# Optimization experiments

Hardware: AMD Instinct MI355X
Metric: run time of the kernel (lower is better)

Reference implementation:

```python
import jax, jax.numpy as jnp
import numpy as np

SMOOTH = 9.0
EPS = 1e-8
LEAK = 0.1  # LeakyReLU slope used by SCAN_attention


def setup_inputs() -> dict:
    key = jax.random.key(0)
    k1, k2, k3, k4 = jax.random.split(key, 4)
    n_img, n_reg, d = 256, 36, 1024
    n_cap, max_w = 256, 60
    imgs = jax.random.normal(k1, (n_img, n_reg, d), dtype=jnp.float32)
    caps = jax.random.normal(k2, (n_cap, max_w, d), dtype=jnp.float32)
    img_lens = jax.random.randint(k3, (n_img,), 1, n_reg + 1, dtype=jnp.int32)
    cap_lens = jax.random.randint(k4, (n_cap,), 5, max_w + 1, dtype=jnp.int32)
    return {"imgs": imgs, "caps": caps, "img_lens": img_lens, "cap_lens": cap_lens}


def reference(imgs, caps, img_lens, cap_lens):
    # imgs: (I, R, D); caps: (C, W, D); cap_lens: (C,)
    C, W, D = caps.shape
    mask = (jnp.arange(W)[None, :] < cap_lens[:, None]).astype(caps.dtype)  # (C, W)
    # Zero padded words: equivalent to the per-caption slicing in the torch loop
    q = caps * mask[:, :, None]

    # SCAN attention, vectorized over captions and images.
    # raw scores: context . query^T  -> (C, I, W, R)
    s = jnp.einsum('cwd,ird->ciwr', q, imgs)
    s = jnp.where(s >= 0, s, LEAK * s)  # LeakyReLU(0.1)
    # l2norm over the word dim (padded words contribute exactly 0)
    norm = jnp.sqrt(jnp.sum(s * s, axis=2, keepdims=True)) + EPS
    s = s / norm
    attn = jax.nn.softmax(s * SMOOTH, axis=3)  # softmax over regions
    wctx = jnp.einsum('ciwr,ird->ciwd', attn, imgs)  # (C, I, W, D)

    # cosine similarity over feature dim
    w12 = jnp.einsum('cwd,ciwd->ciw', q, wctx)
    w1 = jnp.sqrt(jnp.sum(q * q, axis=-1))[:, None, :]          # (C, 1, W)
    w2 = jnp.sqrt(jnp.sum(wctx * wctx, axis=-1))                # (C, I, W)
    sim = w12 / jnp.maximum(w1 * w2, EPS)                       # (C, I, W)

    # masked mean over valid words (matches per-caption mean over n_word)
    col = jnp.sum(sim * mask[:, None, :], axis=2) / cap_lens.astype(sim.dtype)[:, None]
    return col.T  # (n_image, n_caption)
```

## Files before the change

kernel.cpp:

```cpp
#include <hip/hip_runtime.h>


#define NIMG 256
#define NREG 36
#define DIM 1024
#define NCAP 256
#define MAXW 60
#define WPAD 64

typedef short bf16x8 __attribute__((ext_vector_type(8)));
typedef float f32x4 __attribute__((ext_vector_type(4)));

__device__ __forceinline__ unsigned short f2bf(float f) {
  unsigned u = __float_as_uint(f);
  u += 0x7FFF + ((u >> 16) & 1);
  return (unsigned short)(u >> 16);
}

__global__ void k_prep_w1(const float* __restrict__ caps, const int* __restrict__ cap_lens,
                          float* __restrict__ w1) {
  const int bid = blockIdx.x;
  const int c = bid >> 6;
  const int w = bid & 63;
  const int t = threadIdx.x;
  const bool valid = (w < MAXW) && (w < cap_lens[c]);
  float4 v = make_float4(0.f, 0.f, 0.f, 0.f);
  if (valid) v = *reinterpret_cast<const float4*>(caps + ((size_t)c * MAXW + w) * DIM + t * 4);
  float ss = v.x * v.x + v.y * v.y + v.z * v.z + v.w * v.w;
#pragma unroll
  for (int m = 1; m <= 32; m <<= 1) ss += __shfl_xor(ss, m);
  __shared__ float part[4];
  if ((t & 63) == 0) part[t >> 6] = ss;
  __syncthreads();
  if (t == 0) w1[bid] = sqrtf(part[0] + part[1] + part[2] + part[3]);
}

__global__ void k_prep_caps_frag(const float* __restrict__ caps, const int* __restrict__ cap_lens,
                                 unsigned short* __restrict__ qbfF) {
  const int k32 = blockIdx.x;
  const int c = blockIdx.y;
  const int t = threadIdx.x;
  const int mt = t >> 6;
  const int lane = t & 63;
  const int m = mt * 16 + (lane & 15);
  const int k0 = k32 * 32 + (lane >> 4) * 8;
  const int clen = cap_lens[c];
  float4 v0 = make_float4(0.f, 0.f, 0.f, 0.f), v1 = v0;
  if (m < clen && m < MAXW) {
    const float* src = caps + ((size_t)c * MAXW + m) * DIM + k0;
    v0 = *reinterpret_cast<const float4*>(src);
    v1 = *reinterpret_cast<const float4*>(src + 4);
  }
  ushort4 o0, o1;
  o0.x = f2bf(v0.x); o0.y = f2bf(v0.y); o0.z = f2bf(v0.z); o0.w = f2bf(v0.w);
  o1.x = f2bf(v1.x); o1.y = f2bf(v1.y); o1.z = f2bf(v1.z); o1.w = f2bf(v1.w);
  unsigned short* dst = qbfF + ((size_t)(((c * 32 + k32) * 4 + mt) * 64 + lane)) * 8;
  *reinterpret_cast<ushort4*>(dst) = o0;
  *reinterpret_cast<ushort4*>(dst + 4) = o1;
}

__global__ void k_prep_imgs_frag(const float* __restrict__ imgs,
                                 unsigned short* __restrict__ ibfF) {
  const int k32 = blockIdx.x;
  const int i = blockIdx.y;
  const int t = threadIdx.x;
  const int nt = t >> 6;
  const int lane = t & 63;
  const int r = nt * 16 + (lane & 15);
  const int k0 = k32 * 32 + (lane >> 4) * 8;
  float4 v0 = make_float4(0.f, 0.f, 0.f, 0.f), v1 = v0;
  if (r < NREG) {
    const float* src = imgs + ((size_t)i * NREG + r) * DIM + k0;
    v0 = *reinterpret_cast<const float4*>(src);
    v1 = *reinterpret_cast<const float4*>(src + 4);
  }
  ushort4 o0, o1;
  o0.x = f2bf(v0.x); o0.y = f2bf(v0.y); o0.z = f2bf(v0.z); o0.w = f2bf(v0.w);
  o1.x = f2bf(v1.x); o1.y = f2bf(v1.y); o1.z = f2bf(v1.z); o1.w = f2bf(v1.w);
  unsigned short* dst = ibfF + ((size_t)(((i * 32 + k32) * 3 + nt) * 64 + lane)) * 8;
  *reinterpret_cast<ushort4*>(dst) = o0;
  *reinterpret_cast<ushort4*>(dst + 4) = o1;
}

__global__ void k_gram_mfma(const float* __restrict__ imgs,
                            const unsigned short* __restrict__ ibfF,
                            unsigned short* __restrict__ gbf,
                            float* __restrict__ gdiag) {
  const int i = blockIdx.x;
  const int lane = threadIdx.x & 63;
  const int l15 = lane & 15;
  const int quad = lane >> 4;

  float* dg = gdiag + (size_t)i * 48;
#pragma unroll
  for (int r0 = 0; r0 < 36; r0 += 4) {
    const int r = r0 + quad;
    const float* row = imgs + ((size_t)i * NREG + r) * DIM;
    float ss = 0.f;
#pragma unroll
    for (int p = 0; p < 16; ++p) {
      float4 v = *reinterpret_cast<const float4*>(row + p * 64 + l15 * 4);
      ss += v.x * v.x + v.y * v.y + v.z * v.z + v.w * v.w;
    }
    ss += __shfl_xor(ss, 1); ss += __shfl_xor(ss, 2);
    ss += __shfl_xor(ss, 4); ss += __shfl_xor(ss, 8);
    if (l15 == 0) dg[r] = ss;
  }
  if (lane < 12) dg[36 + lane] = 0.f;

  const unsigned short* base = ibfF + ((size_t)i * 32 * 3) * 512 + lane * 8;
  const f32x4 zero4 = {0.f, 0.f, 0.f, 0.f};
  f32x4 acc[3][3];
#pragma unroll
  for (int na = 0; na < 3; ++na)
#pragma unroll
    for (int nb = 0; nb < 3; ++nb) acc[na][nb] = zero4;
  bf16x8 f[2][3];
#pragma unroll
  for (int nt = 0; nt < 3; ++nt)
    f[0][nt] = *reinterpret_cast<const bf16x8*>(base + (size_t)nt * 512);
#pragma unroll
  for (int k32 = 0; k32 < 32; ++k32) {
    if (k32 + 1 < 32) {
      const int nb_ = (k32 + 1) & 1;
#pragma unroll
      for (int nt = 0; nt < 3; ++nt)
        f[nb_][nt] = *reinterpret_cast<const bf16x8*>(base + ((size_t)(k32 + 1) * 3 + nt) * 512);
    }
    const int b = k32 & 1;
#pragma unroll
    for (int na = 0; na < 3; ++na)
#pragma unroll
      for (int nb = 0; nb < 3; ++nb)
        acc[na][nb] = __builtin_amdgcn_mfma_f32_16x16x32_bf16(f[b][na], f[b][nb], acc[na][nb], 0, 0, 0);
  }
  unsigned short* g = gbf + (size_t)i * (48 * 64);
#pragma unroll
  for (int na = 0; na < 3; ++na)
#pragma unroll
    for (int nb = 0; nb < 3; ++nb)
#pragma unroll
      for (int rg = 0; rg < 4; ++rg) {
        const int r = na * 16 + quad * 4 + rg;
        const int c = nb * 16 + l15;
        g[r * 64 + c] = (r == c) ? (unsigned short)0 : f2bf(acc[na][nb][rg]);
      }
  for (int idx = lane; idx < 96; idx += 64) {
    const int r = idx >> 1, half = idx & 1;
    *reinterpret_cast<uint4*>(g + r * 64 + 48 + half * 8) = make_uint4(0, 0, 0, 0);
  }
}

template <int MLIM>
__device__ __forceinline__ void kloopT(const unsigned short* __restrict__ aBase,
                                       const unsigned short* __restrict__ bBase,
                                       f32x4 (&acc)[4][3]) {
  bf16x8 fa[3][MLIM], fb[3][3];
  auto load = [&](int k32, int buf) __attribute__((always_inline)) {
#pragma unroll
    for (int nt = 0; nt < 3; ++nt)
      fb[buf][nt] = *reinterpret_cast<const bf16x8*>(bBase + ((size_t)k32 * 3 + nt) * 512);
#pragma unroll
    for (int mt = 0; mt < MLIM; ++mt)
      fa[buf][mt] = *reinterpret_cast<const bf16x8*>(aBase + ((size_t)k32 * 4 + mt) * 512);
  };
  auto compute = [&](int buf) __attribute__((always_inline)) {
#pragma unroll
    for (int mt = 0; mt < MLIM; ++mt)
#pragma unroll
      for (int nt = 0; nt < 3; ++nt)
        acc[mt][nt] = __builtin_amdgcn_mfma_f32_16x16x32_bf16(fa[buf][mt], fb[buf][nt], acc[mt][nt], 0, 0, 0);
  };
  load(0, 0);
  load(1, 1);
#pragma unroll
  for (int k32 = 0; k32 < 32; ++k32) {
    if (k32 + 2 < 32) load(k32 + 2, (k32 + 2) % 3);
    __builtin_amdgcn_sched_barrier(0);
    compute(k32 % 3);
  }
}

__launch_bounds__(256, 3)
__global__ void k_main(const unsigned short* __restrict__ qbfF,
                       const unsigned short* __restrict__ ibfF,
                       const float* __restrict__ w1,
                       const unsigned short* __restrict__ gbf,
                       const float* __restrict__ gdiag,
                       const int* __restrict__ cap_lens,
                       float* __restrict__ out) {
  __shared__ struct {
    unsigned short attn[4][64 * 64];
    float w12[4][64];
    float w2d[4][64];
    float w2x[4][64];
  } lds;
  const int tid = threadIdx.x;
  const int lane = tid & 63;
  const int wv = tid >> 6;
  const int l15 = lane & 15;
  const int quad = lane >> 4;
  const int flat = blockIdx.y * (NIMG / 2) + blockIdx.x;
  const int xcd = flat & 7;
  const int idx = flat >> 3;
  const int bx = xcd * 16 + (idx & 15);
  const int by = idx >> 4;
  const int i0 = bx * 2;
  const int c = by * 2 + (wv & 1);
  const int img = i0 + (wv >> 1);
  const int clen = cap_lens[c];
  const int mlim = (clen + 15) >> 4;

  f32x4 acc[4][3];
  const f32x4 zero4 = {0.f, 0.f, 0.f, 0.f};
#pragma unroll
  for (int mt = 0; mt < 4; ++mt)
#pragma unroll
    for (int nt = 0; nt < 3; ++nt) acc[mt][nt] = zero4;

  const unsigned short* aBase = qbfF + ((size_t)c * 32 * 4) * 512 + lane * 8;
  const unsigned short* bBase = ibfF + ((size_t)img * 32 * 3) * 512 + lane * 8;

  switch (mlim) {
    case 1: kloopT<1>(aBase, bBase, acc); break;
    case 2: kloopT<2>(aBase, bBase, acc); break;
    case 3: kloopT<3>(aBase, bBase, acc); break;
    default: kloopT<4>(aBase, bBase, acc); break;
  }

  {
    uint4* ab = reinterpret_cast<uint4*>(&lds.attn[wv][0]);
    const uint4 z4 = make_uint4(0, 0, 0, 0);
    for (int j = lane; j < 512; j += 64) ab[j] = z4;
  }

  const int lo = l15 & 7, hi = l15 >> 3;
  const float* dg = gdiag + (size_t)img * 48;
  const float d0 = dg[l15];
  const float d1 = dg[16 + l15];
  const float d2 = dg[32 + l15];

  float scale[3];
#pragma unroll
  for (int nt = 0; nt < 3; ++nt) {
    float p = 0.f;
#pragma unroll
    for (int mt = 0; mt < 4; ++mt)
      if (mt < mlim)
#pragma unroll
        for (int rg = 0; rg < 4; ++rg) {
          float s = acc[mt][nt][rg];
          float l = s < 0.f ? 0.1f * s : s;
          p += l * l;
        }
    p += __shfl_xor(p, 16);
    p += __shfl_xor(p, 32);
    scale[nt] = 9.0f / (sqrtf(p) + 1e-8f);
  }
  const bool vr2 = (l15 < 4);
#pragma unroll
  for (int mt = 0; mt < 4; ++mt) {
    if (mt >= mlim) continue;
#pragma unroll
    for (int rg = 0; rg < 4; ++rg) {
      const float s0 = acc[mt][0][rg];
      const float s1 = acc[mt][1][rg];
      const float s2 = acc[mt][2][rg];
      const float t0 = (s0 < 0.f ? 0.1f * s0 : s0) * scale[0];
      const float t1 = (s1 < 0.f ? 0.1f * s1 : s1) * scale[1];
      const float t2 = (s2 < 0.f ? 0.1f * s2 : s2) * scale[2];
      float mx = fmaxf(t0, t1);
      if (vr2) mx = fmaxf(mx, t2);
      mx = fmaxf(mx, __shfl_xor(mx, 1));
      mx = fmaxf(mx, __shfl_xor(mx, 2));
      mx = fmaxf(mx, __shfl_xor(mx, 4));
      mx = fmaxf(mx, __shfl_xor(mx, 8));
      const float e0 = __expf(t0 - mx);
      const float e1 = __expf(t1 - mx);
      const float e2 = vr2 ? __expf(t2 - mx) : 0.f;
      float sm = e0 + e1 + e2;
      sm += __shfl_xor(sm, 1);
      sm += __shfl_xor(sm, 2);
      sm += __shfl_xor(sm, 4);
      sm += __shfl_xor(sm, 8);
      const float inv = 1.0f / sm;
      const float a0 = e0 * inv, a1 = e1 * inv, a2 = e2 * inv;
      float wp = a0 * s0 + a1 * s1 + a2 * s2;
      float dd = a0 * a0 * d0 + a1 * a1 * d1 + a2 * a2 * d2;
      wp += __shfl_xor(wp, 1); wp += __shfl_xor(wp, 2);
      wp += __shfl_xor(wp, 4); wp += __shfl_xor(wp, 8);
      dd += __shfl_xor(dd, 1); dd += __shfl_xor(dd, 2);
      dd += __shfl_xor(dd, 4); dd += __shfl_xor(dd, 8);
      const int w = mt * 16 + quad * 4 + rg;
      const int w7 = w & 7;
      unsigned short* arow = &lds.attn[wv][w * 64];
      arow[(((0 + hi) ^ w7) << 3) + lo] = f2bf(a0);
      arow[(((2 + hi) ^ w7) << 3) + lo] = f2bf(a1);
      arow[(((4 + hi) ^ w7) << 3) + lo] = f2bf(a2);
      if (l15 == 0) { lds.w12[wv][w] = wp; lds.w2d[wv][w] = dd; }
    }
  }
  bf16x8 gfrag[3][2];
#pragma unroll
  for (int nt = 0; nt < 3; ++nt)
#pragma unroll
    for (int ks = 0; ks < 2; ++ks)
      gfrag[nt][ks] = *reinterpret_cast<const bf16x8*>(
          gbf + ((size_t)img * 48 + nt * 16 + l15) * 64 + ((ks * 4 + quad) << 3));
#pragma unroll
  for (int mt = 0; mt < 4; ++mt) {
    if (mt >= mlim) continue;
    bf16x8 af[2];
#pragma unroll
    for (int ks = 0; ks < 2; ++ks)
      af[ks] = *reinterpret_cast<const bf16x8*>(
          &lds.attn[wv][(mt * 16 + l15) * 64 + (((ks * 4 + quad) ^ (l15 & 7)) << 3)]);
    f32x4 Y[3] = {zero4, zero4, zero4};
#pragma unroll
    for (int nt = 0; nt < 3; ++nt)
#pragma unroll
      for (int ks = 0; ks < 2; ++ks)
        Y[nt] = __builtin_amdgcn_mfma_f32_16x16x32_bf16(af[ks], gfrag[nt][ks], Y[nt], 0, 0, 0);
#pragma unroll
    for (int rg = 0; rg < 4; ++rg) {
      const int w = mt * 16 + quad * 4 + rg;
      const int w7 = w & 7;
      float p = 0.f;
#pragma unroll
      for (int nt = 0; nt < 3; ++nt) {
        const unsigned short b = lds.attn[wv][w * 64 + (((nt * 2 + hi) ^ w7) << 3) + lo];
        p += __uint_as_float((unsigned)b << 16) * Y[nt][rg];
      }
      p += __shfl_xor(p, 1); p += __shfl_xor(p, 2);
      p += __shfl_xor(p, 4); p += __shfl_xor(p, 8);
      if (l15 == 0) lds.w2x[wv][w] = p;
    }
  }
  float simv = 0.f;
  if (lane < clen) {
    const float w2sq = fmaxf(lds.w2x[wv][lane] + lds.w2d[wv][lane], 0.f);
    const float w2v = sqrtf(w2sq);
    const float w12v = lds.w12[wv][lane];
    const float w1v = w1[(size_t)c * WPAD + lane];
    simv = w12v / fmaxf(w1v * w2v, 1e-8f);
  }
  simv += __shfl_xor(simv, 1);
  simv += __shfl_xor(simv, 2);
  simv += __shfl_xor(simv, 4);
  simv += __shfl_xor(simv, 8);
  simv += __shfl_xor(simv, 16);
  simv += __shfl_xor(simv, 32);
  if (lane == 0) out[(size_t)img * NCAP + c] = simv / (float)clen;
}

extern "C" void kernel_launch(void* const* d_in, const int* in_sizes, int n_in,
                              void* d_out, int out_size, void* d_ws, size_t ws_size,
                              hipStream_t stream) {
  const float* imgs = (const float*)d_in[0];
  const float* caps = (const float*)d_in[1];
  const int* cap_lens = (const int*)d_in[3];
  float* out = (float*)d_out;

  char* ws = (char*)d_ws;
  const size_t QBF_B = (size_t)NCAP * 32 * 4 * 512 * 2;
  const size_t IBF_B = (size_t)NIMG * 32 * 3 * 512 * 2;
  const size_t W1_B = (size_t)NCAP * WPAD * 4;
  const size_t GBF_B = (size_t)NIMG * 48 * 64 * 2;
  unsigned short* qbfF = (unsigned short*)ws;
  unsigned short* ibfF = (unsigned short*)(ws + QBF_B);
  float* w1 = (float*)(ws + QBF_B + IBF_B);
  unsigned short* gbf = (unsigned short*)(ws + QBF_B + IBF_B + W1_B);
  float* gdiag = (float*)(ws + QBF_B + IBF_B + W1_B + GBF_B);

  k_prep_w1<<<NCAP * WPAD, 256, 0, stream>>>(caps, cap_lens, w1);
  k_prep_caps_frag<<<dim3(32, NCAP), 256, 0, stream>>>(caps, cap_lens, qbfF);
  k_prep_imgs_frag<<<dim3(32, NIMG), 192, 0, stream>>>(imgs, ibfF);
  k_gram_mfma<<<NIMG, 64, 0, stream>>>(imgs, ibfF, gbf, gdiag);
  k_main<<<dim3(NIMG / 2, NCAP / 2), 256, 0, stream>>>(qbfF, ibfF, w1, gbf, gdiag, cap_lens, out);
}
```

Before: 597.7 us.

## Transpose MFMA operands so softmax over regions runs in-lane with fewer shuffles

```diff
diff --git a/kernel.cpp b/kernel.cpp
--- a/kernel.cpp
+++ b/kernel.cpp
@@ -154,7 +154,7 @@
 template <int MLIM>
 __device__ __forceinline__ void kloopT(const unsigned short* __restrict__ aBase,
                                        const unsigned short* __restrict__ bBase,
-                                       f32x4 (&acc)[4][3]) {
+                                       f32x4 (&acc)[3][4]) {
   bf16x8 fa[3][MLIM], fb[3][3];
   auto load = [&](int k32, int buf) __attribute__((always_inline)) {
 #pragma unroll
@@ -169,7 +169,7 @@
     for (int mt = 0; mt < MLIM; ++mt)
 #pragma unroll
       for (int nt = 0; nt < 3; ++nt)
-        acc[mt][nt] = __builtin_amdgcn_mfma_f32_16x16x32_bf16(fa[buf][mt], fb[buf][nt], acc[mt][nt], 0, 0, 0);
+        acc[nt][mt] = __builtin_amdgcn_mfma_f32_16x16x32_bf16(fb[buf][nt], fa[buf][mt], acc[nt][mt], 0, 0, 0);
   };
   load(0, 0);
   load(1, 1);
@@ -211,12 +211,12 @@
   const int clen = cap_lens[c];
   const int mlim = (clen + 15) >> 4;
 
-  f32x4 acc[4][3];
+  f32x4 acc[3][4];
   const f32x4 zero4 = {0.f, 0.f, 0.f, 0.f};
 #pragma unroll
-  for (int mt = 0; mt < 4; ++mt)
-#pragma unroll
-    for (int nt = 0; nt < 3; ++nt) acc[mt][nt] = zero4;
+  for (int nt = 0; nt < 3; ++nt)
+#pragma unroll
+    for (int mt = 0; mt < 4; ++mt) acc[nt][mt] = zero4;
 
   const unsigned short* aBase = qbfF + ((size_t)c * 32 * 4) * 512 + lane * 8;
   const unsigned short* bBase = ibfF + ((size_t)img * 32 * 3) * 512 + lane * 8;
@@ -234,72 +234,70 @@
     for (int j = lane; j < 512; j += 64) ab[j] = z4;
   }
 
-  const int lo = l15 & 7, hi = l15 >> 3;
   const float* dg = gdiag + (size_t)img * 48;
-  const float d0 = dg[l15];
-  const float d1 = dg[16 + l15];
-  const float d2 = dg[32 + l15];
-
-  float scale[3];
-#pragma unroll
-  for (int nt = 0; nt < 3; ++nt) {
-    float p = 0.f;
-#pragma unroll
-    for (int mt = 0; mt < 4; ++mt)
-      if (mt < mlim)
-#pragma unroll
-        for (int rg = 0; rg < 4; ++rg) {
-          float s = acc[mt][nt][rg];
-          float l = s < 0.f ? 0.1f * s : s;
+  float dv[3][4];
+#pragma unroll
+  for (int nt = 0; nt < 3; ++nt)
+#pragma unroll
+    for (int rg = 0; rg < 4; ++rg)
+      dv[nt][rg] = dg[nt * 16 + quad * 4 + rg];
+
+  float scale[3][4];
+#pragma unroll
+  for (int nt = 0; nt < 3; ++nt)
+#pragma unroll
+    for (int rg = 0; rg < 4; ++rg) {
+      float p = 0.f;
+#pragma unroll
+      for (int mt = 0; mt < 4; ++mt)
+        if (mt < mlim) {
+          const float s = acc[nt][mt][rg];
+          const float l = s < 0.f ? 0.1f * s : s;
           p += l * l;
         }
-    p += __shfl_xor(p, 16);
-    p += __shfl_xor(p, 32);
-    scale[nt] = 9.0f / (sqrtf(p) + 1e-8f);
-  }
-  const bool vr2 = (l15 < 4);
+      p += __shfl_xor(p, 1); p += __shfl_xor(p, 2);
+      p += __shfl_xor(p, 4); p += __shfl_xor(p, 8);
+      scale[nt][rg] = 9.0f / (sqrtf(p) + 1e-8f);
+    }
+
+  float a_all[4][3][4];
+  float inv4[4];
 #pragma unroll
   for (int mt = 0; mt < 4; ++mt) {
     if (mt >= mlim) continue;
-#pragma unroll
-    for (int rg = 0; rg < 4; ++rg) {
-      const float s0 = acc[mt][0][rg];
-      const float s1 = acc[mt][1][rg];
-      const float s2 = acc[mt][2][rg];
-      const float t0 = (s0 < 0.f ? 0.1f * s0 : s0) * scale[0];
-      const float t1 = (s1 < 0.f ? 0.1f * s1 : s1) * scale[1];
-      const float t2 = (s2 < 0.f ? 0.1f * s2 : s2) * scale[2];
-      float mx = fmaxf(t0, t1);
-      if (vr2) mx = fmaxf(mx, t2);
-      mx = fmaxf(mx, __shfl_xor(mx, 1));
-      mx = fmaxf(mx, __shfl_xor(mx, 2));
-      mx = fmaxf(mx, __shfl_xor(mx, 4));
-      mx = fmaxf(mx, __shfl_xor(mx, 8));
-      const float e0 = __expf(t0 - mx);
-      const float e1 = __expf(t1 - mx);
-      const float e2 = vr2 ? __expf(t2 - mx) : 0.f;
-      float sm = e0 + e1 + e2;
-      sm += __shfl_xor(sm, 1);
-      sm += __shfl_xor(sm, 2);
-      sm += __shfl_xor(sm, 4);
-      sm += __shfl_xor(sm, 8);
-      const float inv = 1.0f / sm;
-      const float a0 = e0 * inv, a1 = e1 * inv, a2 = e2 * inv;
-      float wp = a0 * s0 + a1 * s1 + a2 * s2;
-      float dd = a0 * a0 * d0 + a1 * a1 * d1 + a2 * a2 * d2;
-      wp += __shfl_xor(wp, 1); wp += __shfl_xor(wp, 2);
-      wp += __shfl_xor(wp, 4); wp += __shfl_xor(wp, 8);
-      dd += __shfl_xor(dd, 1); dd += __shfl_xor(dd, 2);
-      dd += __shfl_xor(dd, 4); dd += __shfl_xor(dd, 8);
-      const int w = mt * 16 + quad * 4 + rg;
-      const int w7 = w & 7;
-      unsigned short* arow = &lds.attn[wv][w * 64];
-      arow[(((0 + hi) ^ w7) << 3) + lo] = f2bf(a0);
-      arow[(((2 + hi) ^ w7) << 3) + lo] = f2bf(a1);
-      arow[(((4 + hi) ^ w7) << 3) + lo] = f2bf(a2);
-      if (l15 == 0) { lds.w12[wv][w] = wp; lds.w2d[wv][w] = dd; }
+    float sm = 0.f, wp = 0.f, dd = 0.f;
+#pragma unroll
+    for (int nt = 0; nt < 3; ++nt) {
+      const bool rvalid = (nt < 2) || (quad == 0);
+#pragma unroll
+      for (int rg = 0; rg < 4; ++rg) {
+        const float s = acc[nt][mt][rg];
+        const float l = s < 0.f ? 0.1f * s : s;
+        const float ee = rvalid ? __expf(l * scale[nt][rg]) : 0.f;
+        a_all[mt][nt][rg] = ee;
+        sm += ee;
+        wp += ee * s;
+        dd += ee * ee * dv[nt][rg];
+      }
     }
-  }
+    sm += __shfl_xor(sm, 16); sm += __shfl_xor(sm, 32);
+    wp += __shfl_xor(wp, 16); wp += __shfl_xor(wp, 32);
+    dd += __shfl_xor(dd, 16); dd += __shfl_xor(dd, 32);
+    const float inv = 1.0f / sm;
+    inv4[mt] = inv;
+    const int w = mt * 16 + l15;
+    const int key = l15 & 7;
+    unsigned short* arow = &lds.attn[wv][w * 64];
+#pragma unroll
+    for (int nt = 0; nt < 3; ++nt)
+#pragma unroll
+      for (int rg = 0; rg < 4; ++rg) {
+        const int r = nt * 16 + quad * 4 + rg;
+        arow[(((r >> 3) ^ key) << 3) + (r & 7)] = f2bf(a_all[mt][nt][rg] * inv);
+      }
+    if (quad == 0) { lds.w12[wv][w] = wp * inv; lds.w2d[wv][w] = dd * inv * inv; }
+  }
+
   bf16x8 gfrag[3][2];
 #pragma unroll
   for (int nt = 0; nt < 3; ++nt)
@@ -315,27 +313,23 @@
     for (int ks = 0; ks < 2; ++ks)
       af[ks] = *reinterpret_cast<const bf16x8*>(
           &lds.attn[wv][(mt * 16 + l15) * 64 + (((ks * 4 + quad) ^ (l15 & 7)) << 3)]);
-    f32x4 Y[3] = {zero4, zero4, zero4};
+    f32x4 Yt[3] = {zero4, zero4, zero4};
 #pragma unroll
     for (int nt = 0; nt < 3; ++nt)
 #pragma unroll
       for (int ks = 0; ks < 2; ++ks)
-        Y[nt] = __builtin_amdgcn_mfma_f32_16x16x32_bf16(af[ks], gfrag[nt][ks], Y[nt], 0, 0, 0);
-#pragma unroll
-    for (int rg = 0; rg < 4; ++rg) {
-      const int w = mt * 16 + quad * 4 + rg;
-      const int w7 = w & 7;
-      float p = 0.f;
-#pragma unroll
-      for (int nt = 0; nt < 3; ++nt) {
-        const unsigned short b = lds.attn[wv][w * 64 + (((nt * 2 + hi) ^ w7) << 3) + lo];
-        p += __uint_as_float((unsigned)b << 16) * Y[nt][rg];
-      }
-      p += __shfl_xor(p, 1); p += __shfl_xor(p, 2);
-      p += __shfl_xor(p, 4); p += __shfl_xor(p, 8);
-      if (l15 == 0) lds.w2x[wv][w] = p;
-    }
-  }
+        Yt[nt] = __builtin_amdgcn_mfma_f32_16x16x32_bf16(gfrag[nt][ks], af[ks], Yt[nt], 0, 0, 0);
+    float p = 0.f;
+#pragma unroll
+    for (int nt = 0; nt < 3; ++nt)
+#pragma unroll
+      for (int rg = 0; rg < 4; ++rg)
+        p += a_all[mt][nt][rg] * Yt[nt][rg];
+    p *= inv4[mt];
+    p += __shfl_xor(p, 16); p += __shfl_xor(p, 32);
+    if (quad == 0) lds.w2x[wv][mt * 16 + l15] = p;
+  }
+
   float simv = 0.f;
   if (lane < clen) {
     const float w2sq = fmaxf(lds.w2x[wv][lane] + lds.w2d[wv][lane], 0.f);
```

Result: faster. 522.6 us (-12.6%).
